# Performance work log

Measured on AMD Instinct MI355X. Metric: run time of the kernel, lower is better.

## Reference

```python
import jax, jax.numpy as jnp
import numpy as np
from jax import lax

B, C, H, W = 8, 64, 256, 256
K = 10  # num_experts


def conv1x1(x, w):
    # x: [B,C,H,W], w: [O,C] (1x1 conv, no bias)
    return jnp.einsum('oc,bchw->bohw', w, x)


def dyn_conv_se(x, attn, Wk, bk, gamma):
    # Dynamic_conv2d_se with with_se=True, kernel 3, stride 1, pad 1, groups=1.
    # attn: [B,K]; Wk: [K,O,I,3,3]; bk: [K,O]; gamma: [B,O]
    aw = jnp.einsum('bk,koihw->boihw', attn, Wk)        # per-sample kernels
    ab = attn @ bk                                      # [B,O]

    def one(xi, wi):
        # xi: [C,H,W], wi: [O,I,3,3]
        return lax.conv_general_dilated(
            xi[None], wi, window_strides=(1, 1), padding='SAME',
            dimension_numbers=('NCHW', 'OIHW', 'NCHW'))[0]

    y = jax.vmap(one)(x, aw) + ab[:, :, None, None]
    return y * gamma[:, :, None, None]  # SE gain


def setup_inputs() -> dict:
    key = jax.random.key(0)
    ks = jax.random.split(key, 12)
    x = jax.random.normal(ks[0], (B, C, H, W), dtype=jnp.float32)
    logits = jax.random.uniform(ks[1], (B, K), dtype=jnp.float32)
    weights = jax.nn.softmax(logits, axis=-1)
    gamma = jax.random.uniform(ks[2], (B, C), dtype=jnp.float32)
    par = jax.random.uniform(ks[3], (B, 3, 1, H, W), dtype=jnp.float32)
    s = 0.1  # default_init_weights scale
    w1 = jax.random.normal(ks[4], (K, C, C, 3, 3), dtype=jnp.float32) * s
    b1 = jax.random.normal(ks[5], (K, C), dtype=jnp.float32) * 0.01
    w2 = jax.random.normal(ks[6], (K, C, C, 3, 3), dtype=jnp.float32) * s
    b2 = jax.random.normal(ks[7], (K, C), dtype=jnp.float32) * 0.01
    w_16x16 = jax.random.normal(ks[8], (C, C), dtype=jnp.float32) * s
    w_16x8 = jax.random.normal(ks[9], (C, C), dtype=jnp.float32) * s
    w_8x8 = jax.random.normal(ks[10], (C, C), dtype=jnp.float32) * s
    return {'x': x, 'weights': weights, 'gamma': gamma, 'par': par,
            'w1': w1, 'b1': b1, 'w2': w2, 'b2': b2,
            'w_16x16': w_16x16, 'w_16x8': w_16x8, 'w_8x8': w_8x8}


def reference(x, weights, gamma, par, w1, b1, w2, b2, w_16x16, w_16x8, w_8x8):
    # channel_first=True, sparse_val=False, one_layer=False, res_scale=1
    identity = x
    dyres = (conv1x1(x, w_16x16) * par[:, 0]
             + conv1x1(x, w_16x8) * par[:, 1]
             + conv1x1(x, w_8x8) * par[:, 2])
    out = jax.nn.relu(dyn_conv_se(x, weights, w2, b2, gamma) + dyres)
    out = dyn_conv_se(out, weights, w1, b1, gamma)
    return identity + out  # res_scale = 1
```

## Files before the change

### kernel.cpp

```cpp
#include <hip/hip_runtime.h>
#include <hip/hip_bf16.h>

typedef __attribute__((ext_vector_type(8))) short short8;
typedef __attribute__((ext_vector_type(4))) float f32x4;

#define B_ 8
#define C_ 64
#define H_ 256
#define W_ 256
#define HW_ 65536
#define K_ 10
#define NS1 24
#define NS2 18
#define HP_ 258
#define WP_ 258
#define PXP_ (HP_*WP_)
#define SLABW 34
#define SLABR 10

static __device__ __forceinline__ unsigned short f2bf(float f) {
    __hip_bfloat16 hb = __float2bfloat16(f);
    return *(unsigned short*)&hb;
}
static __device__ __forceinline__ float bf2f(unsigned short u) {
    unsigned v = ((unsigned)u) << 16;
    float f;
    __builtin_memcpy(&f, &v, 4);
    return f;
}

static __device__ __forceinline__ void gload_lds16(const void* g, void* l) {
    __builtin_amdgcn_global_load_lds(
        (const __attribute__((address_space(1))) unsigned int*)(unsigned long long)g,
        (__attribute__((address_space(3))) unsigned int*)(unsigned int)(unsigned long long)l,
        16, 0, 0);
}

__global__ void k_combine(const float* __restrict__ attn, const float* __restrict__ gamma,
                          const float* __restrict__ w1, const float* __restrict__ b1,
                          const float* __restrict__ w2, const float* __restrict__ b2,
                          const float* __restrict__ w16, const float* __restrict__ w168,
                          const float* __restrict__ w88,
                          unsigned short* __restrict__ W4_1, unsigned short* __restrict__ W4_2,
                          float* __restrict__ bias1, float* __restrict__ bias2) {
    const int N1 = B_ * NS1 * 2048;
    const int N2 = B_ * NS2 * 2048;
    int gid = blockIdx.x * 256 + threadIdx.x;
    if (gid < N1) {
        int b = gid / (NS1 * 2048);
        int r = gid - b * (NS1 * 2048);
        int s = r >> 11;
        int r2 = r & 2047;
        int of = r2 >> 9, l = (r2 >> 3) & 63, j = r2 & 7;
        int o = of * 16 + (l & 15);
        int g = l >> 4;
        float val;
        if (s < 18) {
            int t = s >> 1, h = s & 1;
            int c = h * 32 + g * 8 + j;
            float acc = 0.f;
            #pragma unroll
            for (int k = 0; k < K_; ++k)
                acc += attn[b * K_ + k] * w2[((size_t)(k * 64 + o) * 64 + c) * 9 + t];
            val = acc * gamma[b * 64 + o];
        } else {
            int e = s - 18;
            int m = e >> 1, h = e & 1;
            int c = h * 32 + g * 8 + j;
            const float* wm = (m == 0) ? w16 : (m == 1 ? w168 : w88);
            val = wm[o * 64 + c];
        }
        W4_1[gid] = f2bf(val);
    } else if (gid < N1 + N2) {
        int gid2 = gid - N1;
        int b = gid2 / (NS2 * 2048);
        int r = gid2 - b * (NS2 * 2048);
        int s = r >> 11;
        int r2 = r & 2047;
        int of = r2 >> 9, l = (r2 >> 3) & 63, j = r2 & 7;
        int o = of * 16 + (l & 15);
        int g = l >> 4;
        int t = s >> 1, h = s & 1;
        int c = h * 32 + g * 8 + j;
        float acc = 0.f;
        #pragma unroll
        for (int k = 0; k < K_; ++k)
            acc += attn[b * K_ + k] * w1[((size_t)(k * 64 + o) * 64 + c) * 9 + t];
        W4_2[gid2] = f2bf(acc * gamma[b * 64 + o]);
    } else if (gid < N1 + N2 + 1024) {
        int id2 = gid - N1 - N2;
        int b = id2 >> 7;
        int rest = id2 & 127;
        int o = rest >> 1;
        int which = rest & 1;
        const float* bb = which ? b1 : b2;
        float acc = 0.f;
        #pragma unroll
        for (int k = 0; k < K_; ++k) acc += attn[b * K_ + k] * bb[k * 64 + o];
        float v = acc * gamma[b * 64 + o];
        if (which) bias2[b * 64 + o] = v; else bias1[b * 64 + o] = v;
    }
}

__global__ void k_border(unsigned short* __restrict__ X1p, unsigned short* __restrict__ Tp) {
    int gid = blockIdx.x * 256 + threadIdx.x;
    if (gid >= 2 * B_ * 1028 * 8) return;
    int chunk = gid & 7;
    int rest = gid >> 3;
    int p = rest % 1028;
    int rb = rest / 1028;
    int buf = rb & 1, b = rb >> 1;
    int row, col;
    if (p < 258) { row = 0; col = p; }
    else if (p < 516) { row = 257; col = p - 258; }
    else if (p < 772) { row = p - 516 + 1; col = 0; }
    else { row = p - 772 + 1; col = 257; }
    unsigned short* base = (buf ? Tp : X1p) +
        ((size_t)b * PXP_ + (size_t)row * WP_ + col) * 64 + chunk * 8;
    *(short8*)base = (short8){0, 0, 0, 0, 0, 0, 0, 0};
}

__global__ __launch_bounds__(256) void k_prep(const float* __restrict__ x,
                                              unsigned short* __restrict__ X1p) {
    __shared__ float ls[64][65];
    const int b = blockIdx.y;
    const int px0 = blockIdx.x * 64;
    const int row = px0 >> 8;
    const int col0 = px0 & 255;
    const int t = threadIdx.x;
    for (int e = t; e < 4096; e += 256) {
        int ch = e >> 6, px = e & 63;
        ls[ch][px] = x[((size_t)b * 64 + ch) * HW_ + px0 + px];
    }
    __syncthreads();
    unsigned short* dst = X1p + ((size_t)b * PXP_ + (size_t)(row + 1) * WP_ + col0 + 1) * 64;
    for (int e = t; e < 4096; e += 256) {
        int ch = e & 63, px = e >> 6;
        dst[(size_t)px * 64 + ch] = f2bf(ls[ch][px]);
    }
}

template<int STAGE>
__global__ __launch_bounds__(256, 2) void k_conv(
    const unsigned short* __restrict__ Xp,
    const float* __restrict__ x_res,
    const float* __restrict__ par,
    const unsigned short* __restrict__ W4,
    const float* __restrict__ bias,
    unsigned short* __restrict__ Tp,
    float* __restrict__ Fout)
{
    constexpr int NS = (STAGE == 1) ? NS1 : NS2;
    constexpr int NPH = NS / 2;
    __shared__ short xs[SLABR * SLABW * 64];
    __shared__ short bring[6 * 2048];

    const int tid = threadIdx.x;
    const int l = tid & 63;
    const int wv = tid >> 6;
    const int b = blockIdx.y;
    const int bswz = (blockIdx.x & 7) * 32 + (blockIdx.x >> 3);
    const int rblk = bswz >> 3;
    const int cblk = bswz & 7;
    const int gh0 = rblk * 8, w0 = cblk * 32;
    const int ln15 = l & 15, g = l >> 4;

    const char* XbP = (const char*)Xp + (size_t)b * PXP_ * 128;
    const unsigned short* Wb = W4 + (size_t)b * (NS * 2048);

    float pvv[3][4];
    if constexpr (STAGE == 1) {
        #pragma unroll
        for (int m = 0; m < 3; ++m)
            #pragma unroll
            for (int mf = 0; mf < 4; ++mf)
                pvv[m][mf] = par[((size_t)b * 3 + m) * HW_ +
                                 (gh0 + 2 * wv + (mf >> 1)) * W_ + w0 + 16 * (mf & 1) + ln15];
    }

    f32x4 acc[4][4];
    #pragma unroll
    for (int mf = 0; mf < 4; ++mf)
        #pragma unroll
        for (int of = 0; of < 4; ++of)
            acc[mf][of] = (f32x4){0.f, 0.f, 0.f, 0.f};

    #pragma unroll
    for (int it = 0; it < 11; ++it) {
        int tau = tid + it * 256;
        if (tau < SLABR * SLABW * 8) {
            int slot = tau & 7;
            int rest = tau >> 3;
            int px = rest % SLABW;
            int row = rest / SLABW;
            int cb = slot ^ (px & 7);
            gload_lds16(XbP + ((size_t)(gh0 + row) * WP_ + (w0 + px)) * 128 + cb * 16,
                        (char*)xs + (size_t)tau * 16);
        }
    }
    auto stage_b = [&](int s) {
        gload_lds16((const char*)Wb + (size_t)s * 4096 + tid * 16,
                    (char*)bring + (s % 6) * 4096 + tid * 16);
    };
    stage_b(0); stage_b(1); stage_b(2); stage_b(3);

    auto aload = [&](int s, short8* d) {
        int dh, dw;
        const int h = s & 1;
        if (STAGE == 1 && s >= 18) { dh = 1; dw = 1; }
        else { const int t = s >> 1; dh = t / 3; dw = t - 3 * dh; }
        #pragma unroll
        for (int mf = 0; mf < 4; ++mf) {
            int idx = 16 * (mf & 1) + ln15 + dw;
            int row = 2 * wv + (mf >> 1) + dh;
            d[mf] = *(const short8*)((const char*)xs + (row * SLABW + idx) * 128 +
                                     ((((h << 2) | g) ^ (idx & 7)) << 4));
        }
    };

    asm volatile("s_waitcnt vmcnt(2)" ::: "memory");
    __builtin_amdgcn_s_barrier();

    #pragma unroll
    for (int p = 0; p < NPH; ++p) {
        const int s0 = 2 * p, s1 = 2 * p + 1;
        const char* r0 = (const char*)bring + (s0 % 6) * 4096 + (size_t)l * 16;
        const char* r1 = (const char*)bring + (s1 % 6) * 4096 + (size_t)l * 16;
        short8 b0[4], b1[4];
        #pragma unroll
        for (int of = 0; of < 4; ++of) {
            b0[of] = *(const short8*)(r0 + of * 1024);
            b1[of] = *(const short8*)(r1 + of * 1024);
        }
        short8 a0[4], a1[4];
        aload(s0, a0);
        aload(s1, a1);
        if (s0 + 4 < NS) stage_b(s0 + 4);
        if (s1 + 4 < NS) stage_b(s1 + 4);
        if (STAGE == 1 && s0 >= 18) {
            const int m = (s0 - 18) >> 1;
            #pragma unroll
            for (int mf = 0; mf < 4; ++mf)
                #pragma unroll
                for (int j = 0; j < 8; ++j) {
                    a0[mf][j] = (short)f2bf(bf2f((unsigned short)a0[mf][j]) * pvv[m][mf]);
                    a1[mf][j] = (short)f2bf(bf2f((unsigned short)a1[mf][j]) * pvv[m][mf]);
                }
        }
        __builtin_amdgcn_s_setprio(1);
        #pragma unroll
        for (int mf = 0; mf < 4; ++mf)
            #pragma unroll
            for (int of = 0; of < 4; ++of)
                acc[mf][of] = __builtin_amdgcn_mfma_f32_16x16x32_bf16(
                    a0[mf], b0[of], acc[mf][of], 0, 0, 0);
        #pragma unroll
        for (int mf = 0; mf < 4; ++mf)
            #pragma unroll
            for (int of = 0; of < 4; ++of)
                acc[mf][of] = __builtin_amdgcn_mfma_f32_16x16x32_bf16(
                    a1[mf], b1[of], acc[mf][of], 0, 0, 0);
        __builtin_amdgcn_s_setprio(0);
        if (p + 1 < NPH) {
            const int rem = NS - (2 * p + 2);
            const int nw = (rem >= 4) ? 2 : (rem - 2 > 0 ? rem - 2 : 0);
            if (nw == 2)      asm volatile("s_waitcnt vmcnt(2)" ::: "memory");
            else if (nw == 1) asm volatile("s_waitcnt vmcnt(1)" ::: "memory");
            else              asm volatile("s_waitcnt vmcnt(0)" ::: "memory");
            __builtin_amdgcn_s_barrier();
        }
    }

    if constexpr (STAGE == 1) {
        __syncthreads();
        unsigned short* tl = (unsigned short*)xs;
        #pragma unroll
        for (int of = 0; of < 4; ++of) {
            int o = of * 16 + ln15;
            float bi = bias[b * 64 + o];
            #pragma unroll
            for (int mf = 0; mf < 4; ++mf) {
                int row_local = 2 * wv + (mf >> 1);
                #pragma unroll
                for (int q = 0; q < 4; ++q) {
                    int px = 16 * (mf & 1) + 4 * g + q;
                    float v = fmaxf(acc[mf][of][q] + bi, 0.f);
                    tl[row_local * 2048 + px * 64 + (o ^ ((px & 7) << 3))] = f2bf(v);
                }
            }
        }
        __syncthreads();
        #pragma unroll
        for (int it = 0; it < 8; ++it) {
            int tau = tid + it * 256;
            int row = tau >> 8;
            int px = (tau >> 3) & 31;
            int j = tau & 7;
            short8 v = *(const short8*)(tl + row * 2048 + px * 64 + ((j ^ (px & 7)) * 8));
            *(short8*)(Tp + ((size_t)b * PXP_ + (size_t)(gh0 + row + 1) * WP_ +
                             (w0 + 1 + px)) * 64 + j * 8) = v;
        }
    } else {
        #pragma unroll
        for (int of = 0; of < 4; ++of) {
            int o = of * 16 + ln15;
            float bi = bias[b * 64 + o];
            #pragma unroll
            for (int mf = 0; mf < 4; ++mf) {
                int gh = gh0 + 2 * wv + (mf >> 1);
                int gw = w0 + 16 * (mf & 1) + g * 4;
                size_t idx = ((size_t)b * 64 + o) * HW_ + gh * W_ + gw;
                f32x4 xv = *(const f32x4*)(x_res + idx);
                f32x4 ov;
                #pragma unroll
                for (int q = 0; q < 4; ++q) ov[q] = xv[q] + acc[mf][of][q] + bi;
                *(f32x4*)(Fout + idx) = ov;
            }
        }
    }
}

extern "C" void kernel_launch(void* const* d_in, const int* in_sizes, int n_in,
                              void* d_out, int out_size, void* d_ws, size_t ws_size,
                              hipStream_t stream) {
    const float* x     = (const float*)d_in[0];
    const float* attn  = (const float*)d_in[1];
    const float* gamma = (const float*)d_in[2];
    const float* par   = (const float*)d_in[3];
    const float* w1    = (const float*)d_in[4];
    const float* b1    = (const float*)d_in[5];
    const float* w2    = (const float*)d_in[6];
    const float* b2    = (const float*)d_in[7];
    const float* w16   = (const float*)d_in[8];
    const float* w168  = (const float*)d_in[9];
    const float* w88   = (const float*)d_in[10];
    float* out = (float*)d_out;

    char* w = (char*)d_ws;
    unsigned short* W4_1 = (unsigned short*)w;
    unsigned short* W4_2 = (unsigned short*)(w + 786432);
    float* bias1 = (float*)(w + 786432 + 589824);
    float* bias2 = (float*)(w + 786432 + 589824 + 2048);
    unsigned short* X1p = (unsigned short*)(w + 1380352);
    unsigned short* Tp  = (unsigned short*)(w + 1380352 + 68161536);

    k_combine<<<dim3(2692), dim3(256), 0, stream>>>(attn, gamma, w1, b1, w2, b2,
                                                    w16, w168, w88, W4_1, W4_2, bias1, bias2);
    k_border<<<dim3(514), dim3(256), 0, stream>>>(X1p, Tp);
    k_prep<<<dim3(1024, 8), dim3(256), 0, stream>>>(x, X1p);

    dim3 grid(256, 8);
    k_conv<1><<<grid, dim3(256), 0, stream>>>(X1p, nullptr, par, W4_1, bias1, Tp, nullptr);
    k_conv<2><<<grid, dim3(256), 0, stream>>>(Tp, x, nullptr, W4_2, bias2, nullptr, out);
}
```

Baseline: 186.4 us.

## Stream conv weights directly into registers instead of an LDS ring

Replaces the LDS ring buffer for the per-sample weight fragments with a triple-buffered register prefetch, where each wave loads its own B fragments from global memory two steps ahead. This removes the per-phase block barriers and the LDS weight traffic, and frees LDS. Launch bounds are raised to three blocks per CU to raise occupancy. The cost is more global/L2 loads, since every wave fetches the weights redundantly, and more register pressure under a tighter register budget, which could cause spills.

```diff
diff --git a/kernel.cpp b/kernel.cpp
--- a/kernel.cpp
+++ b/kernel.cpp
@@ -141,7 +141,7 @@
 }
 
 template<int STAGE>
-__global__ __launch_bounds__(256, 2) void k_conv(
+__global__ __launch_bounds__(256, 3) void k_conv(
     const unsigned short* __restrict__ Xp,
     const float* __restrict__ x_res,
     const float* __restrict__ par,
@@ -151,9 +151,7 @@
     float* __restrict__ Fout)
 {
     constexpr int NS = (STAGE == 1) ? NS1 : NS2;
-    constexpr int NPH = NS / 2;
     __shared__ short xs[SLABR * SLABW * 64];
-    __shared__ short bring[6 * 2048];
 
     const int tid = threadIdx.x;
     const int l = tid & 63;
@@ -198,11 +196,15 @@
                         (char*)xs + (size_t)tau * 16);
         }
     }
-    auto stage_b = [&](int s) {
-        gload_lds16((const char*)Wb + (size_t)s * 4096 + tid * 16,
-                    (char*)bring + (s % 6) * 4096 + tid * 16);
+
+    short8 breg[3][4];
+    auto bload = [&](int s, short8* d) {
+        const unsigned short* wp = Wb + (size_t)s * 2048 + l * 8;
+        #pragma unroll
+        for (int of = 0; of < 4; ++of) d[of] = *(const short8*)(wp + of * 512);
     };
-    stage_b(0); stage_b(1); stage_b(2); stage_b(3);
+    bload(0, breg[0]);
+    bload(1, breg[1]);
 
     auto aload = [&](int s, short8* d) {
         int dh, dw;
@@ -218,34 +220,25 @@
         }
     };
 
-    asm volatile("s_waitcnt vmcnt(2)" ::: "memory");
+    asm volatile("s_waitcnt vmcnt(0)" ::: "memory");
     __builtin_amdgcn_s_barrier();
 
     #pragma unroll
-    for (int p = 0; p < NPH; ++p) {
-        const int s0 = 2 * p, s1 = 2 * p + 1;
-        const char* r0 = (const char*)bring + (s0 % 6) * 4096 + (size_t)l * 16;
-        const char* r1 = (const char*)bring + (s1 % 6) * 4096 + (size_t)l * 16;
-        short8 b0[4], b1[4];
-        #pragma unroll
-        for (int of = 0; of < 4; ++of) {
-            b0[of] = *(const short8*)(r0 + of * 1024);
-            b1[of] = *(const short8*)(r1 + of * 1024);
-        }
-        short8 a0[4], a1[4];
-        aload(s0, a0);
-        aload(s1, a1);
-        if (s0 + 4 < NS) stage_b(s0 + 4);
-        if (s1 + 4 < NS) stage_b(s1 + 4);
-        if (STAGE == 1 && s0 >= 18) {
-            const int m = (s0 - 18) >> 1;
+    for (int s = 0; s < NS; ++s) {
+        if (s >= 2) {
+            if (s == NS - 1) asm volatile("s_waitcnt vmcnt(0)" ::: "memory");
+            else             asm volatile("s_waitcnt vmcnt(4)" ::: "memory");
+        }
+        if (s + 2 < NS) bload(s + 2, breg[(s + 2) % 3]);
+        short8 a[4];
+        aload(s, a);
+        if (STAGE == 1 && s >= 18) {
+            const int m = (s - 18) >> 1;
             #pragma unroll
             for (int mf = 0; mf < 4; ++mf)
                 #pragma unroll
-                for (int j = 0; j < 8; ++j) {
-                    a0[mf][j] = (short)f2bf(bf2f((unsigned short)a0[mf][j]) * pvv[m][mf]);
-                    a1[mf][j] = (short)f2bf(bf2f((unsigned short)a1[mf][j]) * pvv[m][mf]);
-                }
+                for (int j = 0; j < 8; ++j)
+                    a[mf][j] = (short)f2bf(bf2f((unsigned short)a[mf][j]) * pvv[m][mf]);
         }
         __builtin_amdgcn_s_setprio(1);
         #pragma unroll
@@ -253,22 +246,8 @@
             #pragma unroll
             for (int of = 0; of < 4; ++of)
                 acc[mf][of] = __builtin_amdgcn_mfma_f32_16x16x32_bf16(
-                    a0[mf], b0[of], acc[mf][of], 0, 0, 0);
-        #pragma unroll
-        for (int mf = 0; mf < 4; ++mf)
-            #pragma unroll
-            for (int of = 0; of < 4; ++of)
-                acc[mf][of] = __builtin_amdgcn_mfma_f32_16x16x32_bf16(
-                    a1[mf], b1[of], acc[mf][of], 0, 0, 0);
+                    a[mf], breg[s % 3][of], acc[mf][of], 0, 0, 0);
         __builtin_amdgcn_s_setprio(0);
-        if (p + 1 < NPH) {
-            const int rem = NS - (2 * p + 2);
-            const int nw = (rem >= 4) ? 2 : (rem - 2 > 0 ? rem - 2 : 0);
-            if (nw == 2)      asm volatile("s_waitcnt vmcnt(2)" ::: "memory");
-            else if (nw == 1) asm volatile("s_waitcnt vmcnt(1)" ::: "memory");
-            else              asm volatile("s_waitcnt vmcnt(0)" ::: "memory");
-            __builtin_amdgcn_s_barrier();
-        }
     }
 
     if constexpr (STAGE == 1) {
```

Measured after the change: 239.3 us. 28.4% more time.

## Deepen weight ring to eight slots and double-buffer LDS operand reads

Applied to the files above, without the earlier changes.

The shared-memory ring for the per-sample weight slices grows from six to eight slots, and global prefetch now runs six steps ahead instead of four. The A and B operand fragments for the next phase are read from LDS into a second register set while the current phase's MFMAs run. The `vmcnt` wait counts are recomputed to match the new prefetch distance. The aim is to hide LDS read latency and global load latency behind matrix math, at the cost of more VGPRs and 4 KB more LDS per block, which could reduce occupancy or cause spills.

```diff
diff --git a/kernel.cpp b/kernel.cpp
--- a/kernel.cpp
+++ b/kernel.cpp
@@ -153,7 +153,7 @@
     constexpr int NS = (STAGE == 1) ? NS1 : NS2;
     constexpr int NPH = NS / 2;
     __shared__ short xs[SLABR * SLABW * 64];
-    __shared__ short bring[6 * 2048];
+    __shared__ short bring[8 * 2048];
 
     const int tid = threadIdx.x;
     const int l = tid & 63;
@@ -200,9 +200,9 @@
     }
     auto stage_b = [&](int s) {
         gload_lds16((const char*)Wb + (size_t)s * 4096 + tid * 16,
-                    (char*)bring + (s % 6) * 4096 + tid * 16);
+                    (char*)bring + (s & 7) * 4096 + tid * 16);
     };
-    stage_b(0); stage_b(1); stage_b(2); stage_b(3);
+    stage_b(0); stage_b(1); stage_b(2); stage_b(3); stage_b(4); stage_b(5);
 
     auto aload = [&](int s, short8* d) {
         int dh, dw;
@@ -217,26 +217,36 @@
                                      ((((h << 2) | g) ^ (idx & 7)) << 4));
         }
     };
+    auto bread = [&](int s, short8* d) {
+        const char* rb = (const char*)bring + (s & 7) * 4096 + (size_t)l * 16;
+        #pragma unroll
+        for (int of = 0; of < 4; ++of) d[of] = *(const short8*)(rb + of * 1024);
+    };
 
     asm volatile("s_waitcnt vmcnt(2)" ::: "memory");
     __builtin_amdgcn_s_barrier();
+
+    short8 aa[2][8], bb[2][8];
+    aload(0, &aa[0][0]);
+    aload(1, &aa[0][4]);
+    bread(0, &bb[0][0]);
+    bread(1, &bb[0][4]);
 
     #pragma unroll
     for (int p = 0; p < NPH; ++p) {
         const int s0 = 2 * p, s1 = 2 * p + 1;
-        const char* r0 = (const char*)bring + (s0 % 6) * 4096 + (size_t)l * 16;
-        const char* r1 = (const char*)bring + (s1 % 6) * 4096 + (size_t)l * 16;
-        short8 b0[4], b1[4];
-        #pragma unroll
-        for (int of = 0; of < 4; ++of) {
-            b0[of] = *(const short8*)(r0 + of * 1024);
-            b1[of] = *(const short8*)(r1 + of * 1024);
+        const int cur = p & 1, nxt = (p + 1) & 1;
+        if (s0 + 6 < NS) stage_b(s0 + 6);
+        if (s1 + 6 < NS) stage_b(s1 + 6);
+        if (p + 1 < NPH) {
+            aload(s0 + 2, &aa[nxt][0]);
+            aload(s1 + 2, &aa[nxt][4]);
+            bread(s0 + 2, &bb[nxt][0]);
+            bread(s1 + 2, &bb[nxt][4]);
         }
         short8 a0[4], a1[4];
-        aload(s0, a0);
-        aload(s1, a1);
-        if (s0 + 4 < NS) stage_b(s0 + 4);
-        if (s1 + 4 < NS) stage_b(s1 + 4);
+        #pragma unroll
+        for (int mf = 0; mf < 4; ++mf) { a0[mf] = aa[cur][mf]; a1[mf] = aa[cur][4 + mf]; }
         if (STAGE == 1 && s0 >= 18) {
             const int m = (s0 - 18) >> 1;
             #pragma unroll
@@ -253,17 +263,18 @@
             #pragma unroll
             for (int of = 0; of < 4; ++of)
                 acc[mf][of] = __builtin_amdgcn_mfma_f32_16x16x32_bf16(
-                    a0[mf], b0[of], acc[mf][of], 0, 0, 0);
+                    a0[mf], bb[cur][of], acc[mf][of], 0, 0, 0);
         #pragma unroll
         for (int mf = 0; mf < 4; ++mf)
             #pragma unroll
             for (int of = 0; of < 4; ++of)
                 acc[mf][of] = __builtin_amdgcn_mfma_f32_16x16x32_bf16(
-                    a1[mf], b1[of], acc[mf][of], 0, 0, 0);
+                    a1[mf], bb[cur][4 + of], acc[mf][of], 0, 0, 0);
         __builtin_amdgcn_s_setprio(0);
         if (p + 1 < NPH) {
-            const int rem = NS - (2 * p + 2);
-            const int nw = (rem >= 4) ? 2 : (rem - 2 > 0 ? rem - 2 : 0);
+            const int issued = (2 * p + 8 < NS) ? 2 * p + 8 : NS;
+            const int nw0 = issued - (2 * p + 6);
+            const int nw = nw0 < 0 ? 0 : nw0;
             if (nw == 2)      asm volatile("s_waitcnt vmcnt(2)" ::: "memory");
             else if (nw == 1) asm volatile("s_waitcnt vmcnt(1)" ::: "memory");
             else              asm volatile("s_waitcnt vmcnt(0)" ::: "memory");
```

Result: no change. 186.4 us (-0.0%).
